# Kernel tuning notes

Measured on AMD Instinct MI355X. Metric: run time of the kernel, lower is better.

## Reference

```python
import jax, jax.numpy as jnp
import numpy as np

N_NODES = 100000
N_EDGES = 1600000
IN_C = 64
HID = 64


def _glorot(key, shape):
    fan_in, fan_out = shape[1], shape[0]
    lim = (6.0 / (fan_in + fan_out)) ** 0.5
    return jax.random.uniform(key, shape, jnp.float32, -lim, lim)


def setup_inputs() -> dict:
    key = jax.random.key(0)
    ks = jax.random.split(key, 8)
    x = jax.random.normal(ks[0], (N_NODES, IN_C), jnp.float32)
    edge_index = jax.random.randint(ks[1], (2, N_EDGES), 0, N_NODES, jnp.int32)
    return {
        "x": x,
        "edge_index": edge_index,
        # conv1 (SAGEConv in->hid): lin_l (bias), lin_r (no bias)
        "W1l": _glorot(ks[2], (HID, IN_C)),
        "b1l": jnp.zeros((HID,), jnp.float32),
        "W1r": _glorot(ks[3], (HID, IN_C)),
        # conv2 (SAGEConv hid->hid)
        "W2l": _glorot(ks[4], (HID, HID)),
        "b2l": jnp.zeros((HID,), jnp.float32),
        "W2r": _glorot(ks[5], (HID, HID)),
        # edge scorer: Linear(2*hid, 1)
        "Wlin": _glorot(ks[6], (1, 2 * HID)),
        "blin": jnp.zeros((1,), jnp.float32),
    }


def _sage_conv(x, src, dst, Wl, bl, Wr, n_nodes):
    # mean aggregation of source features onto destination nodes
    agg = jax.ops.segment_sum(x[src], dst, num_segments=n_nodes)  # [N, F]
    cnt = jax.ops.segment_sum(jnp.ones((src.shape[0],), x.dtype), dst,
                              num_segments=n_nodes)  # [N]
    mean = agg / jnp.maximum(cnt, 1.0)[:, None]  # isolated nodes -> 0
    return mean @ Wl.T + bl + x @ Wr.T


def reference(x, edge_index, W1l, b1l, W1r, W2l, b2l, W2r, Wlin, blin):
    src, dst = edge_index[0], edge_index[1]
    n = x.shape[0]
    h = jax.nn.relu(_sage_conv(x, src, dst, W1l, b1l, W1r, n))
    h = jax.nn.relu(_sage_conv(h, src, dst, W2l, b2l, W2r, n))
    he = jnp.concatenate([h[src], h[dst]], axis=1)  # [E, 2*HID]
    return (he @ Wlin.T + blin).squeeze(-1)  # [E]
```

## Files before the change

kernel.cpp:

```cpp
#include <hip/hip_runtime.h>
#include <hip/hip_bf16.h>

#define N_NODES 100000
#define N_EDGES 1600000
#define NBUCK 196
#define BCAP 12288
#define CHUNK 4096
#define PART_BLOCKS 391
#define XGROUPS 1600000
#define MSTRIDE 36


typedef __hip_bfloat16 bf16;
typedef short short8 __attribute__((ext_vector_type(8)));
typedef float f32x4 __attribute__((ext_vector_type(4)));
typedef unsigned int uint;

__device__ __forceinline__ short f2bs(float f) {
    bf16 h = __float2bfloat16(f);
    short s; __builtin_memcpy(&s, &h, 2); return s;
}
__device__ __forceinline__ float lo_bf(uint w) {
    uint v = w << 16; float f; __builtin_memcpy(&f, &v, 4); return f;
}
__device__ __forceinline__ float hi_bf(uint w) {
    uint v = w & 0xFFFF0000u; float f; __builtin_memcpy(&f, &v, 4); return f;
}
__device__ __forceinline__ uint pack2(float a, float b) {
    return (uint)(unsigned short)f2bs(a) | ((uint)(unsigned short)f2bs(b) << 16);
}
__device__ __forceinline__ short8 load8bf(const bf16* __restrict__ p, long idx) {
    return *(const short8*)((const short*)p + idx);
}

__global__ __launch_bounds__(256) void partition_kernel(
    const float* __restrict__ x, bf16* __restrict__ xb,
    const float* __restrict__ W1l, const float* __restrict__ W1r,
    const float* __restrict__ W2l, const float* __restrict__ W2r,
    bf16* __restrict__ wb,
    const int* __restrict__ src, const int* __restrict__ dst,
    int* __restrict__ gcur, int* __restrict__ pk)
{
    __shared__ int h[256], scn[256], cur[256], gb[256];
    __shared__ int pl[CHUNK];
    __shared__ unsigned char bb[CHUNK];
    int t = threadIdx.x;
    h[t] = 0;
    {
        int g0 = blockIdx.x * 4096;
        int gend = g0 + 4096 < XGROUPS ? g0 + 4096 : XGROUPS;
        for (int i = g0 + t; i < gend; i += 256) {
            float4 v = ((const float4*)x)[i];
            uint2 o;
            o.x = pack2(v.x, v.y);
            o.y = pack2(v.z, v.w);
            ((uint2*)xb)[i] = o;
        }
        if (blockIdx.x == 0) {
            for (int k = t; k < 16384; k += 256) {
                float v;
                if (k < 4096)       v = W1l[k];
                else if (k < 8192)  v = W1r[k - 4096];
                else if (k < 12288) v = W2l[k - 8192];
                else                v = W2r[k - 12288];
                wb[k] = __float2bfloat16(v);
            }
        }
    }
    __syncthreads();
    int e0 = blockIdx.x * CHUNK;
    for (int i = t; i < CHUNK; i += 256) {
        int e = e0 + i;
        if (e < N_EDGES) atomicAdd(&h[dst[e] >> 9], 1);
    }
    __syncthreads();
    if (t < 64) {
        int v0 = h[t * 4], v1 = h[t * 4 + 1], v2 = h[t * 4 + 2], v3 = h[t * 4 + 3];
        int i0 = v0, i1 = i0 + v1, i2 = i1 + v2, i3 = i2 + v3;
        int run = i3;
#pragma unroll
        for (int off = 1; off < 64; off <<= 1) {
            int u = __shfl_up(run, off);
            if (t >= off) run += u;
        }
        int excl = run - i3;
        scn[t * 4]     = excl + i0;
        scn[t * 4 + 1] = excl + i1;
        scn[t * 4 + 2] = excl + i2;
        scn[t * 4 + 3] = excl + i3;
    }
    __syncthreads();
    cur[t] = scn[t] - h[t];
    __syncthreads();
    int cnt_local = scn[255];
    for (int i = t; i < CHUNK; i += 256) {
        int e = e0 + i;
        if (e < N_EDGES) {
            int d = dst[e];
            int b = d >> 9;
            int p = atomicAdd(&cur[b], 1);
            pl[p] = src[e] | ((d & 511) << 17);
            bb[p] = (unsigned char)b;
        }
    }
    __syncthreads();
    if (h[t] > 0) gb[t] = t * BCAP + atomicAdd(&gcur[t], h[t]);
    __syncthreads();
    for (int i = t; i < cnt_local; i += 256) {
        int b = bb[i];
        int pos = gb[b] + (i - (scn[b] - h[b]));
        if (pos < (b + 1) * BCAP) pk[pos] = pl[i];
    }
}

__global__ __launch_bounds__(512) void csr_build(
    const int* __restrict__ gcur, const int* __restrict__ pk,
    int* __restrict__ csr, int2* __restrict__ node_range)
{
    __shared__ int deg[512], scn[512], cur[512];
    __shared__ int csr_l[BCAP];
    int t = threadIdx.x;
    int b = blockIdx.x;
    int base = b * BCAP;
    int cnt = gcur[b];
    if (cnt > BCAP) cnt = BCAP;
    deg[t] = 0;
    __syncthreads();
    for (int i = t; i < cnt; i += 512)
        atomicAdd(&deg[pk[base + i] >> 17], 1);
    __syncthreads();
    if (t < 64) {
        int e[8], inc[8], s = 0;
#pragma unroll
        for (int k = 0; k < 8; k++) { e[k] = deg[t * 8 + k]; s += e[k]; inc[k] = s; }
        int run = s;
#pragma unroll
        for (int off = 1; off < 64; off <<= 1) {
            int u = __shfl_up(run, off);
            if (t >= off) run += u;
        }
        int excl = run - s;
#pragma unroll
        for (int k = 0; k < 8; k++) scn[t * 8 + k] = excl + inc[k];
    }
    __syncthreads();
    int excl = scn[t] - deg[t];
    cur[t] = excl;
    int n = (b << 9) + t;
    if (n < N_NODES) node_range[n] = make_int2(base + excl, base + excl + deg[t]);
    __syncthreads();
    for (int i = t; i < cnt; i += 512) {
        int v = pk[base + i];
        int p = atomicAdd(&cur[v >> 17], 1);
        csr_l[p] = v & 0x1FFFF;
    }
    __syncthreads();
    for (int i = t; i < cnt; i += 512)
        csr[base + i] = csr_l[i];
}


__device__ __forceinline__ void gather_mean_lds(
    const bf16* __restrict__ feat, const int2* __restrict__ node_range,
    const int* __restrict__ csr, int nb0, uint* __restrict__ mean_l)
{
    int wave = threadIdx.x >> 6, lane = threadIdx.x & 63;
    int g = lane >> 3, ci = lane & 7;
    int nl = wave * 8 + g;
    int n = nb0 + nl;
    int2 rg = (n < N_NODES) ? node_range[n] : make_int2(0, 0);
    int beg = rg.x, end = rg.y;
    const uint* fw = (const uint*)feat;
    float a0 = 0.f, a1 = 0.f, a2 = 0.f, a3 = 0.f;
    float a4 = 0.f, a5 = 0.f, a6 = 0.f, a7 = 0.f;
    int i = beg;
    for (; i + 7 < end; i += 8) {
        int s0 = csr[i],     s1 = csr[i + 1], s2 = csr[i + 2], s3 = csr[i + 3];
        int s4 = csr[i + 4], s5 = csr[i + 5], s6 = csr[i + 6], s7 = csr[i + 7];
        uint4 w0 = *(const uint4*)(fw + (long)s0 * 32 + ci * 4);
        uint4 w1 = *(const uint4*)(fw + (long)s1 * 32 + ci * 4);
        uint4 w2 = *(const uint4*)(fw + (long)s2 * 32 + ci * 4);
        uint4 w3 = *(const uint4*)(fw + (long)s3 * 32 + ci * 4);
        uint4 w4 = *(const uint4*)(fw + (long)s4 * 32 + ci * 4);
        uint4 w5 = *(const uint4*)(fw + (long)s5 * 32 + ci * 4);
        uint4 w6 = *(const uint4*)(fw + (long)s6 * 32 + ci * 4);
        uint4 w7 = *(const uint4*)(fw + (long)s7 * 32 + ci * 4);
        a0 += lo_bf(w0.x) + lo_bf(w1.x) + lo_bf(w2.x) + lo_bf(w3.x)
            + lo_bf(w4.x) + lo_bf(w5.x) + lo_bf(w6.x) + lo_bf(w7.x);
        a1 += hi_bf(w0.x) + hi_bf(w1.x) + hi_bf(w2.x) + hi_bf(w3.x)
            + hi_bf(w4.x) + hi_bf(w5.x) + hi_bf(w6.x) + hi_bf(w7.x);
        a2 += lo_bf(w0.y) + lo_bf(w1.y) + lo_bf(w2.y) + lo_bf(w3.y)
            + lo_bf(w4.y) + lo_bf(w5.y) + lo_bf(w6.y) + lo_bf(w7.y);
        a3 += hi_bf(w0.y) + hi_bf(w1.y) + hi_bf(w2.y) + hi_bf(w3.y)
            + hi_bf(w4.y) + hi_bf(w5.y) + hi_bf(w6.y) + hi_bf(w7.y);
        a4 += lo_bf(w0.z) + lo_bf(w1.z) + lo_bf(w2.z) + lo_bf(w3.z)
            + lo_bf(w4.z) + lo_bf(w5.z) + lo_bf(w6.z) + lo_bf(w7.z);
        a5 += hi_bf(w0.z) + hi_bf(w1.z) + hi_bf(w2.z) + hi_bf(w3.z)
            + hi_bf(w4.z) + hi_bf(w5.z) + hi_bf(w6.z) + hi_bf(w7.z);
        a6 += lo_bf(w0.w) + lo_bf(w1.w) + lo_bf(w2.w) + lo_bf(w3.w)
            + lo_bf(w4.w) + lo_bf(w5.w) + lo_bf(w6.w) + lo_bf(w7.w);
        a7 += hi_bf(w0.w) + hi_bf(w1.w) + hi_bf(w2.w) + hi_bf(w3.w)
            + hi_bf(w4.w) + hi_bf(w5.w) + hi_bf(w6.w) + hi_bf(w7.w);
    }
    for (; i + 1 < end; i += 2) {
        int s0 = csr[i], s1 = csr[i + 1];
        uint4 w0 = *(const uint4*)(fw + (long)s0 * 32 + ci * 4);
        uint4 w1 = *(const uint4*)(fw + (long)s1 * 32 + ci * 4);
        a0 += lo_bf(w0.x) + lo_bf(w1.x); a1 += hi_bf(w0.x) + hi_bf(w1.x);
        a2 += lo_bf(w0.y) + lo_bf(w1.y); a3 += hi_bf(w0.y) + hi_bf(w1.y);
        a4 += lo_bf(w0.z) + lo_bf(w1.z); a5 += hi_bf(w0.z) + hi_bf(w1.z);
        a6 += lo_bf(w0.w) + lo_bf(w1.w); a7 += hi_bf(w0.w) + hi_bf(w1.w);
    }
    if (i < end) {
        int s = csr[i];
        uint4 w = *(const uint4*)(fw + (long)s * 32 + ci * 4);
        a0 += lo_bf(w.x); a1 += hi_bf(w.x);
        a2 += lo_bf(w.y); a3 += hi_bf(w.y);
        a4 += lo_bf(w.z); a5 += hi_bf(w.z);
        a6 += lo_bf(w.w); a7 += hi_bf(w.w);
    }
    int d = end - beg;
    float inv = d > 0 ? 1.0f / (float)d : 0.0f;
    uint4 q;
    q.x = pack2(a0 * inv, a1 * inv);
    q.y = pack2(a2 * inv, a3 * inv);
    q.z = pack2(a4 * inv, a5 * inv);
    q.w = pack2(a6 * inv, a7 * inv);
    *(uint4*)(mean_l + nl * MSTRIDE + ci * 4) = q;
}

__device__ __forceinline__ short8 load_bfrag(
    const bf16* __restrict__ wlb, int f, int c, int quad)
{
    if (c < 2) return load8bf(wlb, (long)f * 64 + c * 32 + quad * 8);
    return load8bf(wlb, 4096 + (long)f * 64 + (c - 2) * 32 + quad * 8);
}

__global__ __launch_bounds__(512) void layer1_fused(
    const bf16* __restrict__ xb, const int2* __restrict__ nrng,
    const int* __restrict__ csr, const bf16* __restrict__ wlb,
    const float* __restrict__ bl, bf16* __restrict__ h_out)
{
    __shared__ uint mean_l[64 * MSTRIDE];
    int nb0 = blockIdx.x * 64;
    gather_mean_lds(xb, nrng, csr, nb0, mean_l);
    __syncthreads();
    int tid = threadIdx.x;
    int wave = tid >> 6, lane = tid & 63;
    if (wave >= 4) return;
    int quad = lane >> 4, n16 = lane & 15;
    int nb = nb0 + wave * 16;
    int ln = wave * 16 + n16;

    int node_a = nb + n16;
    int na = node_a < N_NODES ? node_a : N_NODES - 1;
    short8 a[4];
#pragma unroll
    for (int c = 0; c < 2; c++)
        a[c] = *(const short8*)(mean_l + ln * MSTRIDE + c * 16 + quad * 4);
#pragma unroll
    for (int c = 0; c < 2; c++)
        a[2 + c] = load8bf(xb, (long)na * 64 + c * 32 + quad * 8);

#pragma unroll
    for (int t = 0; t < 4; t++) {
        int f = 16 * t + n16;
        f32x4 acc = {0.f, 0.f, 0.f, 0.f};
#pragma unroll
        for (int c = 0; c < 4; c++) {
            short8 b = load_bfrag(wlb, f, c, quad);
            acc = __builtin_amdgcn_mfma_f32_16x16x32_bf16(a[c], b, acc, 0, 0, 0);
        }
        float bias = bl[f];
#pragma unroll
        for (int r = 0; r < 4; r++) {
            int node = nb + quad * 4 + r;
            if (node < N_NODES)
                h_out[(long)node * 64 + f] = __float2bfloat16(fmaxf(acc[r] + bias, 0.0f));
        }
    }
}

__global__ __launch_bounds__(512) void layer2_fused(
    const bf16* __restrict__ h1, const int2* __restrict__ nrng,
    const int* __restrict__ csr, const bf16* __restrict__ wlb,
    const float* __restrict__ bl, const float* __restrict__ Wlin,
    float* __restrict__ s_src, float* __restrict__ s_dst)
{
    __shared__ uint mean_l[64 * MSTRIDE];
    int nb0 = blockIdx.x * 64;
    gather_mean_lds(h1, nrng, csr, nb0, mean_l);
    __syncthreads();
    int tid = threadIdx.x;
    int wave = tid >> 6, lane = tid & 63;
    if (wave >= 4) return;
    int quad = lane >> 4, n16 = lane & 15;
    int nb = nb0 + wave * 16;
    int ln = wave * 16 + n16;

    int node_a = nb + n16;
    int na = node_a < N_NODES ? node_a : N_NODES - 1;
    short8 a[4];
#pragma unroll
    for (int c = 0; c < 2; c++)
        a[c] = *(const short8*)(mean_l + ln * MSTRIDE + c * 16 + quad * 4);
#pragma unroll
    for (int c = 0; c < 2; c++)
        a[2 + c] = load8bf(h1, (long)na * 64 + c * 32 + quad * 8);

    float sa[4] = {0.f, 0.f, 0.f, 0.f};
    float sb[4] = {0.f, 0.f, 0.f, 0.f};
#pragma unroll
    for (int t = 0; t < 4; t++) {
        int f = 16 * t + n16;
        f32x4 acc = {0.f, 0.f, 0.f, 0.f};
#pragma unroll
        for (int c = 0; c < 4; c++) {
            short8 b = load_bfrag(wlb, f, c, quad);
            acc = __builtin_amdgcn_mfma_f32_16x16x32_bf16(a[c], b, acc, 0, 0, 0);
        }
        float bias = bl[f];
        float wa = Wlin[f];
        float wb = Wlin[64 + f];
#pragma unroll
        for (int r = 0; r < 4; r++) {
            float h = fmaxf(acc[r] + bias, 0.0f);
            sa[r] += h * wa;
            sb[r] += h * wb;
        }
    }
#pragma unroll
    for (int m = 1; m < 16; m <<= 1) {
#pragma unroll
        for (int r = 0; r < 4; r++) {
            sa[r] += __shfl_xor(sa[r], m);
            sb[r] += __shfl_xor(sb[r], m);
        }
    }
    if (n16 == 0) {
#pragma unroll
        for (int r = 0; r < 4; r++) {
            int node = nb + quad * 4 + r;
            if (node < N_NODES) { s_src[node] = sa[r]; s_dst[node] = sb[r]; }
        }
    }
}

__global__ __launch_bounds__(256) void edge_out_kernel(
    const int* __restrict__ src, const int* __restrict__ dst,
    const float* __restrict__ s_src, const float* __restrict__ s_dst,
    const float* __restrict__ blin, float* __restrict__ out)
{
    int i = blockIdx.x * 256 + threadIdx.x;
    if (i >= N_EDGES / 4) return;
    int4 s4 = ((const int4*)src)[i];
    int4 d4 = ((const int4*)dst)[i];
    float b = blin[0];
    float4 o;
    o.x = s_src[s4.x] + s_dst[d4.x] + b;
    o.y = s_src[s4.y] + s_dst[d4.y] + b;
    o.z = s_src[s4.z] + s_dst[d4.z] + b;
    o.w = s_src[s4.w] + s_dst[d4.w] + b;
    ((float4*)out)[i] = o;
}

extern "C" void kernel_launch(void* const* d_in, const int* in_sizes, int n_in,
                              void* d_out, int out_size, void* d_ws, size_t ws_size,
                              hipStream_t stream) {
    const float* x    = (const float*)d_in[0];
    const int*   ei   = (const int*)d_in[1];
    const float* W1l  = (const float*)d_in[2];
    const float* b1l  = (const float*)d_in[3];
    const float* W1r  = (const float*)d_in[4];
    const float* W2l  = (const float*)d_in[5];
    const float* b2l  = (const float*)d_in[6];
    const float* W2r  = (const float*)d_in[7];
    const float* Wlin = (const float*)d_in[8];
    const float* blin = (const float*)d_in[9];
    float* out = (float*)d_out;

    const int* src = ei;
    const int* dst = ei + N_EDGES;

    char* w = (char*)d_ws;
    bf16*  xb    = (bf16*)w;  w += (size_t)N_NODES * 64 * 2;
    bf16*  h1    = (bf16*)w;  w += (size_t)N_NODES * 64 * 2;
    float* ssrc  = (float*)w; w += (size_t)N_NODES * 4;
    float* sdst  = (float*)w; w += (size_t)N_NODES * 4;
    int2*  nrng  = (int2*)w;  w += (size_t)N_NODES * 8;
    int*   gcur  = (int*)w;   w += 256 * 4;
    bf16*  wb    = (bf16*)w;  w += 16384 * 2;
    int*   pk    = (int*)w;   w += (size_t)NBUCK * BCAP * 4;
    int*   csr   = (int*)w;   w += (size_t)NBUCK * BCAP * 4;

    const int fused_blocks = (N_NODES + 63) / 64;
    const int eo_blocks    = (N_EDGES / 4 + 255) / 256;

    (void)hipMemsetAsync(gcur, 0, 256 * 4, stream);
    partition_kernel<<<PART_BLOCKS, 256, 0, stream>>>(
        x, xb, W1l, W1r, W2l, W2r, wb, src, dst, gcur, pk);
    csr_build<<<NBUCK, 512, 0, stream>>>(gcur, pk, csr, nrng);

    layer1_fused<<<fused_blocks, 512, 0, stream>>>(xb, nrng, csr, wb, b1l, h1);
    layer2_fused<<<fused_blocks, 512, 0, stream>>>(h1, nrng, csr, wb + 8192, b2l, Wlin, ssrc, sdst);

    edge_out_kernel<<<eo_blocks, 256, 0, stream>>>(src, dst, ssrc, sdst, blin, out);
}
```

Before: 240.1 us.

## Split x conversion into separate blocks, simplify partition, quarter CSR build per bucket

New measurement: 235.0 us. 1.02x faster.

```diff
diff --git a/kernel.cpp b/kernel.cpp
--- a/kernel.cpp
+++ b/kernel.cpp
@@ -7,7 +7,10 @@
 #define BCAP 12288
 #define CHUNK 4096
 #define PART_BLOCKS 391
-#define XGROUPS 1600000
+#define CONV_BLOCKS 6250
+#define CAP32 32
+#define QNODES 128
+#define QCAP 3072
 #define MSTRIDE 36
 
 
@@ -33,7 +36,7 @@
     return *(const short8*)((const short*)p + idx);
 }
 
-__global__ __launch_bounds__(256) void partition_kernel(
+__global__ __launch_bounds__(256) void prep_kernel(
     const float* __restrict__ x, bf16* __restrict__ xb,
     const float* __restrict__ W1l, const float* __restrict__ W1r,
     const float* __restrict__ W2l, const float* __restrict__ W2r,
@@ -41,75 +44,63 @@
     const int* __restrict__ src, const int* __restrict__ dst,
     int* __restrict__ gcur, int* __restrict__ pk)
 {
-    __shared__ int h[256], scn[256], cur[256], gb[256];
-    __shared__ int pl[CHUNK];
-    __shared__ unsigned char bb[CHUNK];
+    __shared__ int pl[256 * CAP32];
+    __shared__ int cnt[256], gb[256];
     int t = threadIdx.x;
-    h[t] = 0;
-    {
-        int g0 = blockIdx.x * 4096;
-        int gend = g0 + 4096 < XGROUPS ? g0 + 4096 : XGROUPS;
-        for (int i = g0 + t; i < gend; i += 256) {
-            float4 v = ((const float4*)x)[i];
-            uint2 o;
-            o.x = pack2(v.x, v.y);
-            o.y = pack2(v.z, v.w);
-            ((uint2*)xb)[i] = o;
-        }
-        if (blockIdx.x == 0) {
+
+    if (blockIdx.x >= PART_BLOCKS) {
+        int cb = blockIdx.x - PART_BLOCKS;
+        int i = cb * 256 + t;
+        float4 v = ((const float4*)x)[i];
+        uint2 o;
+        o.x = pack2(v.x, v.y);
+        o.y = pack2(v.z, v.w);
+        ((uint2*)xb)[i] = o;
+        if (cb == 0) {
             for (int k = t; k < 16384; k += 256) {
-                float v;
-                if (k < 4096)       v = W1l[k];
-                else if (k < 8192)  v = W1r[k - 4096];
-                else if (k < 12288) v = W2l[k - 8192];
-                else                v = W2r[k - 12288];
-                wb[k] = __float2bfloat16(v);
+                float vv;
+                if (k < 4096)       vv = W1l[k];
+                else if (k < 8192)  vv = W1r[k - 4096];
+                else if (k < 12288) vv = W2l[k - 8192];
+                else                vv = W2r[k - 12288];
+                wb[k] = __float2bfloat16(vv);
             }
         }
-    }
+        return;
+    }
+
+    cnt[t] = 0;
     __syncthreads();
     int e0 = blockIdx.x * CHUNK;
-    for (int i = t; i < CHUNK; i += 256) {
-        int e = e0 + i;
-        if (e < N_EDGES) atomicAdd(&h[dst[e] >> 9], 1);
-    }
-    __syncthreads();
-    if (t < 64) {
-        int v0 = h[t * 4], v1 = h[t * 4 + 1], v2 = h[t * 4 + 2], v3 = h[t * 4 + 3];
-        int i0 = v0, i1 = i0 + v1, i2 = i1 + v2, i3 = i2 + v3;
-        int run = i3;
-#pragma unroll
-        for (int off = 1; off < 64; off <<= 1) {
-            int u = __shfl_up(run, off);
-            if (t >= off) run += u;
-        }
-        int excl = run - i3;
-        scn[t * 4]     = excl + i0;
-        scn[t * 4 + 1] = excl + i1;
-        scn[t * 4 + 2] = excl + i2;
-        scn[t * 4 + 3] = excl + i3;
-    }
-    __syncthreads();
-    cur[t] = scn[t] - h[t];
-    __syncthreads();
-    int cnt_local = scn[255];
     for (int i = t; i < CHUNK; i += 256) {
         int e = e0 + i;
         if (e < N_EDGES) {
             int d = dst[e];
             int b = d >> 9;
-            int p = atomicAdd(&cur[b], 1);
-            pl[p] = src[e] | ((d & 511) << 17);
-            bb[p] = (unsigned char)b;
-        }
-    }
-    __syncthreads();
-    if (h[t] > 0) gb[t] = t * BCAP + atomicAdd(&gcur[t], h[t]);
-    __syncthreads();
-    for (int i = t; i < cnt_local; i += 256) {
-        int b = bb[i];
-        int pos = gb[b] + (i - (scn[b] - h[b]));
-        if (pos < (b + 1) * BCAP) pk[pos] = pl[i];
+            int payload = src[e] | ((d & 511) << 17);
+            int p = atomicAdd(&cnt[b], 1);
+            if (p < CAP32) {
+                pl[b * CAP32 + p] = payload;
+            } else {
+                int g = atomicAdd(&gcur[b], 1);
+                if (g < BCAP) pk[b * BCAP + g] = payload;
+            }
+        }
+    }
+    __syncthreads();
+    {
+        int c = cnt[t] < CAP32 ? cnt[t] : CAP32;
+        gb[t] = c > 0 ? atomicAdd(&gcur[t], c) : 0;
+        cnt[t] = c;
+    }
+    __syncthreads();
+    for (int i = t; i < 256 * CAP32; i += 256) {
+        int b = i >> 5;
+        int pos = i & (CAP32 - 1);
+        if (pos < cnt[b]) {
+            int g = gb[b] + pos;
+            if (g < BCAP) pk[b * BCAP + g] = pl[i];
+        }
     }
 }
 
@@ -117,10 +108,12 @@
     const int* __restrict__ gcur, const int* __restrict__ pk,
     int* __restrict__ csr, int2* __restrict__ node_range)
 {
-    __shared__ int deg[512], scn[512], cur[512];
-    __shared__ int csr_l[BCAP];
+    __shared__ int deg[512], scn[512];
+    __shared__ int cur[QNODES];
+    __shared__ int csr_l[QCAP];
     int t = threadIdx.x;
-    int b = blockIdx.x;
+    int b = blockIdx.x >> 2;
+    int q = blockIdx.x & 3;
     int base = b * BCAP;
     int cnt = gcur[b];
     if (cnt > BCAP) cnt = BCAP;
@@ -144,19 +137,29 @@
         for (int k = 0; k < 8; k++) scn[t * 8 + k] = excl + inc[k];
     }
     __syncthreads();
+    int hs = q * QNODES;
+    int hend = hs + QNODES;
+    int hs_excl = scn[hs] - deg[hs];
+    int he_excl = (hend < 512) ? (scn[hend] - deg[hend]) : cnt;
+    int qcnt = he_excl - hs_excl;
     int excl = scn[t] - deg[t];
-    cur[t] = excl;
-    int n = (b << 9) + t;
-    if (n < N_NODES) node_range[n] = make_int2(base + excl, base + excl + deg[t]);
+    if (t >= hs && t < hend) {
+        cur[t - hs] = excl - hs_excl;
+        int n = (b << 9) + t;
+        if (n < N_NODES) node_range[n] = make_int2(base + excl, base + excl + deg[t]);
+    }
     __syncthreads();
     for (int i = t; i < cnt; i += 512) {
         int v = pk[base + i];
-        int p = atomicAdd(&cur[v >> 17], 1);
-        csr_l[p] = v & 0x1FFFF;
-    }
-    __syncthreads();
-    for (int i = t; i < cnt; i += 512)
-        csr[base + i] = csr_l[i];
+        int ld = v >> 17;
+        if (ld >= hs && ld < hend) {
+            int p = atomicAdd(&cur[ld - hs], 1);
+            if (p < QCAP) csr_l[p] = v & 0x1FFFF;
+        }
+    }
+    __syncthreads();
+    for (int i = t; i < qcnt && i < QCAP; i += 512)
+        csr[base + hs_excl + i] = csr_l[i];
 }
 
 
@@ -221,12 +224,12 @@
     }
     int d = end - beg;
     float inv = d > 0 ? 1.0f / (float)d : 0.0f;
-    uint4 q;
-    q.x = pack2(a0 * inv, a1 * inv);
-    q.y = pack2(a2 * inv, a3 * inv);
-    q.z = pack2(a4 * inv, a5 * inv);
-    q.w = pack2(a6 * inv, a7 * inv);
-    *(uint4*)(mean_l + nl * MSTRIDE + ci * 4) = q;
+    uint4 qv;
+    qv.x = pack2(a0 * inv, a1 * inv);
+    qv.y = pack2(a2 * inv, a3 * inv);
+    qv.z = pack2(a4 * inv, a5 * inv);
+    qv.w = pack2(a6 * inv, a7 * inv);
+    *(uint4*)(mean_l + nl * MSTRIDE + ci * 4) = qv;
 }
 
 __device__ __forceinline__ short8 load_bfrag(
@@ -393,13 +396,15 @@
     int*   pk    = (int*)w;   w += (size_t)NBUCK * BCAP * 4;
     int*   csr   = (int*)w;   w += (size_t)NBUCK * BCAP * 4;
 
+    const int prep_blocks  = PART_BLOCKS + CONV_BLOCKS;
+    const int csr_blocks   = NBUCK * 4;
     const int fused_blocks = (N_NODES + 63) / 64;
     const int eo_blocks    = (N_EDGES / 4 + 255) / 256;
 
     (void)hipMemsetAsync(gcur, 0, 256 * 4, stream);
-    partition_kernel<<<PART_BLOCKS, 256, 0, stream>>>(
+    prep_kernel<<<prep_blocks, 256, 0, stream>>>(
         x, xb, W1l, W1r, W2l, W2r, wb, src, dst, gcur, pk);
-    csr_build<<<NBUCK, 512, 0, stream>>>(gcur, pk, csr, nrng);
+    csr_build<<<csr_blocks, 512, 0, stream>>>(gcur, pk, csr, nrng);
 
     layer1_fused<<<fused_blocks, 512, 0, stream>>>(xb, nrng, csr, wb, b1l, h1);
     layer2_fused<<<fused_blocks, 512, 0, stream>>>(h1, nrng, csr, wb + 8192, b2l, Wlin, ssrc, sdst);
```
